# Kernel tuning notes

Hardware: AMD Instinct MI355X
Metric: run time of the kernel (lower is better)

The kernel has to match this reference:

```python
import jax, jax.numpy as jnp
import numpy as np

DT = 0.1       # time separation between grid points (forward dt arg default)
UT = 0.1       # stationary-mode time constant
K_IN, K_OUT, K_STATE = 8, 4, 128
PRE_LEN, FWD_LEN, BATCH = 64, 128, 4096


def setup_inputs() -> dict:
    key = jax.random.key(0)
    ks = jax.random.split(key, 16)
    H = K_STATE
    s = 0.05  # small init keeps the 128-step integration numerically tame
    d = {}
    d['pre_x'] = jax.random.normal(ks[0], (PRE_LEN, BATCH, K_IN), jnp.float32)
    d['pre_y'] = jax.random.normal(ks[1], (PRE_LEN, BATCH, K_OUT), jnp.float32)
    d['forward_x'] = jax.random.normal(ks[2], (FWD_LEN, BATCH, K_IN), jnp.float32)
    # encoder nn.GRU (1 layer), torch gate order r,z,n
    d['W_ih'] = jax.random.normal(ks[3], (3 * H, K_IN + K_OUT), jnp.float32) * s
    d['W_hh'] = jax.random.normal(ks[4], (3 * H, H), jnp.float32) * s
    d['b_ih'] = jax.random.normal(ks[5], (3 * H,), jnp.float32) * s
    d['b_hh'] = jax.random.normal(ks[6], (3 * H,), jnp.float32) * s
    # expand_input: Linear(k_in, k_state) + Tanh
    d['W_e'] = jax.random.normal(ks[7], (H, K_IN), jnp.float32) * s
    d['b_e'] = jax.random.normal(ks[8], (H,), jnp.float32) * s
    # ODE GRU cell (BasicCell with net_type='GRU'): input size = k_state
    d['Wc_ih'] = jax.random.normal(ks[9], (3 * H, H), jnp.float32) * s
    d['Wc_hh'] = jax.random.normal(ks[10], (3 * H, H), jnp.float32) * s
    d['bc_ih'] = jax.random.normal(ks[11], (3 * H,), jnp.float32) * s
    d['bc_hh'] = jax.random.normal(ks[12], (3 * H,), jnp.float32) * s
    # fc: Linear(H, 2H, bias=False) -> Tanh -> Linear(2H, k_out, bias=False)
    d['W1'] = jax.random.normal(ks[13], (2 * H, H), jnp.float32) * s
    d['W2'] = jax.random.normal(ks[14], (K_OUT, 2 * H), jnp.float32) * s
    return d


def _gru_cell(x, h, Wi, Wh, bi, bh):
    gi = x @ Wi.T + bi
    gh = h @ Wh.T + bh
    ir, iz, inn = jnp.split(gi, 3, axis=-1)
    hr, hz, hn = jnp.split(gh, 3, axis=-1)
    r = jax.nn.sigmoid(ir + hr)
    z = jax.nn.sigmoid(iz + hz)
    n = jnp.tanh(inn + r * hn)
    return (1.0 - z) * n + z * h


def reference(pre_x, pre_y, forward_x, W_ih, W_hh, b_ih, b_hh, W_e, b_e,
              Wc_ih, Wc_hh, bc_ih, bc_hh, W1, W2):
    H = W_hh.shape[1]
    # ---- GRU encoder over [pre_x, pre_y], take final hidden state ----
    enc_in = jnp.concatenate([pre_x, pre_y], axis=2)  # [Tp, B, k_in+k_out]
    h0 = jnp.zeros((enc_in.shape[1], H), enc_in.dtype)

    def enc_step(h, x):
        return _gru_cell(x, h, W_ih, W_hh, b_ih, b_hh), None

    hn, _ = jax.lax.scan(enc_step, h0, enc_in)  # [B, H]

    # ---- natural cubic spline of the control input over the grid ----
    L = forward_x.shape[0]
    hs = DT
    ys = jnp.concatenate([pre_x[-1:], forward_x], axis=0)  # [L+1, B, k_in]
    rhs = 6.0 * (ys[:-2] - 2.0 * ys[1:-1] + ys[2:]) / (hs * hs)  # [L-1, ...]
    nin = L - 1
    A = 4.0 * jnp.eye(nin) + jnp.eye(nin, k=1) + jnp.eye(nin, k=-1)
    Minner = jnp.linalg.solve(A, rhs.reshape(nin, -1)).reshape(rhs.shape)
    zpad = jnp.zeros_like(ys[:1])
    M = jnp.concatenate([zpad, Minner, zpad], axis=0)  # 2nd derivs, [L+1,B,k_in]

    def u(t):
        i = jnp.clip(jnp.floor(t / hs).astype(jnp.int32), 0, L - 1)
        t0 = i.astype(ys.dtype) * hs
        a = (t0 + hs - t) / hs
        b = (t - t0) / hs
        yi, yi1 = jnp.take(ys, i, axis=0), jnp.take(ys, i + 1, axis=0)
        Mi, Mi1 = jnp.take(M, i, axis=0), jnp.take(M, i + 1, axis=0)
        return a * yi + b * yi1 + ((a ** 3 - a) * Mi + (b ** 3 - b) * Mi1) * (hs * hs) / 6.0

    # ---- ODE system: stationary GRU-cell dynamics ----
    def f(t, y):
        x = jnp.tanh(u(t) @ W_e.T + b_e)
        return (_gru_cell(x, y, Wc_ih, Wc_hh, bc_ih, bc_hh) - y) / UT

    # ---- fixed-grid RK4 (torchdiffeq method='rk4', one step per interval) ----
    def rk4(y, t0):
        k1 = f(t0, y)
        k2 = f(t0 + hs / 2, y + (hs / 2) * k1)
        k3 = f(t0 + hs / 2, y + (hs / 2) * k2)
        k4 = f(t0 + hs, y + hs * k3)
        yn = y + (hs / 6.0) * (k1 + 2 * k2 + 2 * k3 + k4)
        return yn, yn

    t_starts = jnp.arange(L, dtype=ys.dtype) * hs
    _, traj = jax.lax.scan(rk4, hn, t_starts)  # [L, B, H]

    # ---- output head: Linear -> Tanh -> Linear (no bias) ----
    return jnp.tanh(traj @ W1.T) @ W2.T  # [L, B, k_out]
```

## Files before the change

### kernel.cpp

```cpp
#include <hip/hip_runtime.h>
#include <math.h>

#define NB    4096
#define NH    128
#define NKIN  8
#define NKOUT 4
#define NTP   64
#define NL    128
#define BKIN  (NB*NKIN)

typedef __attribute__((ext_vector_type(8))) short short8;
typedef __attribute__((ext_vector_type(4))) float f32x4;

__device__ __forceinline__ short f2bf(float f) {
    union { float f; unsigned u; } v; v.f = f;
    unsigned u = v.u;
    unsigned r = (u + 0x7fffu + ((u >> 16) & 1u)) >> 16;
    return (short)r;
}
__device__ __forceinline__ float sigf(float x)   { return __builtin_amdgcn_rcpf(1.0f + __expf(-x)); }
__device__ __forceinline__ float tanhf_(float x) { return 1.0f - 2.0f*__builtin_amdgcn_rcpf(1.0f + __expf(2.0f*x)); }

__global__ void spline_um_kernel(const float* __restrict__ pre_x,
                                 const float* __restrict__ fx,
                                 float* __restrict__ UM)
{
    __shared__ float cp[128];
    if (threadIdx.x == 0) {
        float c = 0.f;
        for (int j = 1; j <= 127; ++j) { c = 1.0f/(4.0f - c); cp[j] = c; }
    }
    __syncthreads();
    int col = blockIdx.x*256 + threadIdx.x;
    const float r6 = 6.0f/(0.1f*0.1f);
    const float KK = 0.01f/16.0f;
    float y0 = pre_x[(size_t)(NTP-1)*BKIN + col];
    float y1 = fx[col];
    float d = 0.f;
    for (int j = 1; j <= 127; ++j) {
        float y2 = fx[(size_t)j*BKIN + col];
        float r  = r6*(y0 - 2.f*y1 + y2);
        d = (r - d)*cp[j];
        UM[(size_t)j*BKIN + col] = d;
        y0 = y1; y1 = y2;
    }
    float xn  = 0.f;
    float yj1 = fx[(size_t)127*BKIN + col];
    for (int j = 127; j >= 1; --j) {
        float dj = UM[(size_t)j*BKIN + col];
        float x  = dj - cp[j]*xn;
        float yj = fx[(size_t)(j-1)*BKIN + col];
        UM[(size_t)j*BKIN + col] = 0.5f*(yj + yj1) - KK*(x + xn);
        xn = x; yj1 = yj;
    }
    float ys0 = pre_x[(size_t)(NTP-1)*BKIN + col];
    UM[col] = 0.5f*(ys0 + yj1) - KK*xn;
}

__global__ void prep_frags(const float* __restrict__ W1, const float* __restrict__ W2,
                           short* __restrict__ w1f, short* __restrict__ w2f)
{
    int tid = threadIdx.x;
    for (int idx = tid; idx < 16*4*64*8; idx += 256) {
        int j = idx & 7, lane = (idx >> 3) & 63, fc = idx >> 9;
        int t = fc >> 2, c = fc & 3;
        int n = t*16 + (lane & 15);
        int k = c*32 + (lane >> 4)*8 + j;
        w1f[idx] = f2bf(W1[n*NH + k]);
    }
    for (int idx = tid; idx < 8*64*8; idx += 256) {
        int j = idx & 7, lane = (idx >> 3) & 63, c = idx >> 9;
        int m = lane & 15;
        int k = c*32 + (lane >> 4)*8 + j;
        w2f[idx] = (m < NKOUT) ? f2bf(W2[m*2*NH + k]) : (short)0;
    }
}

__device__ __forceinline__ void gemm12(const short* base, const short8 (&B)[3][4], f32x4 (&c)[3])
{
    #pragma unroll
    for (int kc = 0; kc < 4; ++kc) {
        short8 a = *(const short8*)(base + kc*32);
        #pragma unroll
        for (int g = 0; g < 3; ++g)
            c[g] = __builtin_amdgcn_mfma_f32_16x16x32_bf16(a, B[g][kc], c[g], 0, 0, 0);
    }
}

__device__ __forceinline__ void writeA(short* buf, int stride, int col, int quad, f32x4 v)
{
    #pragma unroll
    for (int r = 0; r < 4; ++r) buf[(quad*4 + r)*stride + col] = f2bf(v[r]);
}

__device__ __forceinline__ void gateK(const f32x4 (&gi)[3], const f32x4 (&gh)[3],
                                      const f32x4& yin, float brz, float bzz,
                                      float bin_, float bhn_, f32x4& K)
{
    #pragma unroll
    for (int r = 0; r < 4; ++r) {
        float rg = sigf(gi[0][r] + gh[0][r] + brz);
        float zg = sigf(gi[1][r] + gh[1][r] + bzz);
        float ng = tanhf_(gi[2][r] + bin_ + rg*(gh[2][r] + bhn_));
        K[r] = (1.0f - zg)*(ng - yin[r]);
    }
}

__global__ void __launch_bounds__(512, 2)
fused_kernel(const float* __restrict__ pre_x, const float* __restrict__ pre_y,
             const float* __restrict__ fx,
             const float* __restrict__ W_ih, const float* __restrict__ W_hh,
             const float* __restrict__ b_ih, const float* __restrict__ b_hh,
             const float* __restrict__ W_e,  const float* __restrict__ b_e,
             const float* __restrict__ Wc_ih,const float* __restrict__ Wc_hh,
             const float* __restrict__ bc_ih,const float* __restrict__ bc_hh,
             const float* __restrict__ UM,   const short* __restrict__ w1f,
             const short* __restrict__ w2f,  float* __restrict__ out)
{
    __shared__ __align__(16) short Yb [16*136];
    __shared__ __align__(16) short E0 [16*136];
    __shared__ __align__(16) short E1 [16*136];
    __shared__ __align__(16) short XMb[16*136];
    __shared__ __align__(16) short X1b[16*136];
    __shared__ __align__(16) short UMb[16*40];
    __shared__ __align__(16) short U1b[16*40];
    __shared__ __align__(16) short OB [16*264];

    const int tid  = threadIdx.x;
    const int w    = tid >> 6;
    const int lane = tid & 63;
    const int quad = lane >> 4;
    const int m    = lane & 15;
    const int hcol = w*16 + m;
    const int b0   = blockIdx.x * 16;
    const f32x4 z4 = {0.f, 0.f, 0.f, 0.f};

    for (int i = tid; i < 2176; i += 512) Yb[i] = 0;
    for (int i = tid; i < 640;  i += 512) { UMb[i] = 0; U1b[i] = 0; }

    short8 Bhh[3][4], Bih_c[3][4];
    #pragma unroll
    for (int g = 0; g < 3; ++g)
        #pragma unroll
        for (int c = 0; c < 4; ++c) {
            int n = g*NH + hcol, kb = c*32 + quad*8;
            short8 f1, f2;
            #pragma unroll
            for (int j = 0; j < 8; ++j) {
                f1[j] = f2bf(Wc_hh[n*NH + kb + j]);
                f2[j] = f2bf(Wc_ih[n*NH + kb + j]);
            }
            Bhh[g][c] = f1; Bih_c[g][c] = f2;
        }
    short8 Ehh[3][4];
    #pragma unroll
    for (int g = 0; g < 3; ++g)
        #pragma unroll
        for (int c = 0; c < 4; ++c) {
            int n = g*NH + hcol, kb = c*32 + quad*8;
            short8 f1;
            #pragma unroll
            for (int j = 0; j < 8; ++j) f1[j] = f2bf(W_hh[n*NH + kb + j]);
            Ehh[g][c] = f1;
        }
    short8 Eih[3];
    #pragma unroll
    for (int g = 0; g < 3; ++g) {
        short8 f1;
        #pragma unroll
        for (int j = 0; j < 8; ++j) {
            int k = quad*8 + j;
            f1[j] = (k < 12) ? f2bf(W_ih[(g*NH + hcol)*12 + k]) : (short)0;
        }
        Eih[g] = f1;
    }
    short8 Bexp;
    #pragma unroll
    for (int j = 0; j < 8; ++j) {
        int k = quad*8 + j;
        Bexp[j] = (k < NKIN) ? f2bf(W_e[hcol*NKIN + k]) : (short)0;
    }
    const float be   = b_e[hcol];
    const float brz  = bc_ih[hcol]        + bc_hh[hcol];
    const float bzz  = bc_ih[NH + hcol]   + bc_hh[NH + hcol];
    const float bin_ = bc_ih[2*NH + hcol];
    const float bhn_ = bc_hh[2*NH + hcol];
    const float erz  = b_ih[hcol]         + b_hh[hcol];
    const float ezz  = b_ih[NH + hcol]    + b_hh[NH + hcol];
    const float ein_ = b_ih[2*NH + hcol];
    const float ehn_ = b_hh[2*NH + hcol];

    f32x4 y = z4;

    const int eb = tid / 12, ek = tid - eb*12;
    float encv = 0.f;
    if (tid < 192)
        encv = (ek < NKIN) ? pre_x[((size_t)0*NB + b0 + eb)*NKIN + ek]
                           : pre_y[((size_t)0*NB + b0 + eb)*NKOUT + (ek - NKIN)];
    __syncthreads();
    for (int t = 0; t < NTP; ++t) {
        if (tid < 192) {
            UMb[eb*40 + ek] = f2bf(encv);
            if (t + 1 < NTP)
                encv = (ek < NKIN) ? pre_x[((size_t)(t+1)*NB + b0 + eb)*NKIN + ek]
                                   : pre_y[((size_t)(t+1)*NB + b0 + eb)*NKOUT + (ek - NKIN)];
        }
        __syncthreads();
        f32x4 gi[3] = {z4, z4, z4};
        {
            short8 a = *(const short8*)(UMb + m*40 + quad*8);
            #pragma unroll
            for (int g = 0; g < 3; ++g)
                gi[g] = __builtin_amdgcn_mfma_f32_16x16x32_bf16(a, Eih[g], gi[g], 0, 0, 0);
        }
        f32x4 gh[3] = {z4, z4, z4};
        gemm12(Yb + m*136 + quad*8, Ehh, gh);
        f32x4 K;
        gateK(gi, gh, y, erz, ezz, ein_, ehn_, K);
        #pragma unroll
        for (int r = 0; r < 4; ++r) y[r] += K[r];
        __syncthreads();
        writeA(Yb, 136, hcol, quad, y);
    }
    if (tid < 64) UMb[(tid >> 2)*40 + 8 + (tid & 3)] = 0;

    const int sb = tid >> 3, sk = tid & 7;
    const size_t scol = (size_t)(b0 + sb)*NKIN + sk;
    if (tid < 128) UMb[sb*40 + sk] = f2bf(pre_x[(size_t)(NTP-1)*BKIN + scol]);
    __syncthreads();
    f32x4 gi0[3] = {z4, z4, z4};
    {
        short8 a = *(const short8*)(UMb + m*40 + quad*8);
        f32x4 c0 = z4;
        c0 = __builtin_amdgcn_mfma_f32_16x16x32_bf16(a, Bexp, c0, 0, 0, 0);
        f32x4 xv;
        #pragma unroll
        for (int r = 0; r < 4; ++r) xv[r] = tanhf_(c0[r] + be);
        writeA(XMb, 136, hcol, quad, xv);
    }
    __syncthreads();
    gemm12(XMb + m*136 + quad*8, Bih_c, gi0);

    float fxv = 0.f, umv = 0.f;
    if (tid < 128) { fxv = fx[scol]; umv = UM[scol]; }

    const short8* W1F = (const short8*)w1f;
    const short8* W2F = (const short8*)w2f;

    for (int st = 0; st < NL; ++st) {
        if (tid < 128) {
            U1b[sb*40 + sk] = f2bf(fxv);
            UMb[sb*40 + sk] = f2bf(umv);
        }
        __syncthreads();
        f32x4 xmv, x1v;
        {
            short8 am = *(const short8*)(UMb + m*40 + quad*8);
            short8 a1 = *(const short8*)(U1b + m*40 + quad*8);
            f32x4 cm = z4, c1 = z4;
            cm = __builtin_amdgcn_mfma_f32_16x16x32_bf16(am, Bexp, cm, 0, 0, 0);
            c1 = __builtin_amdgcn_mfma_f32_16x16x32_bf16(a1, Bexp, c1, 0, 0, 0);
            #pragma unroll
            for (int r = 0; r < 4; ++r) {
                xmv[r] = tanhf_(cm[r] + be);
                x1v[r] = tanhf_(c1[r] + be);
            }
        }
        writeA(XMb, 136, hcol, quad, xmv);
        writeA(X1b, 136, hcol, quad, x1v);
        if (tid < 128 && st + 1 < NL) {
            fxv = fx[(size_t)(st+1)*BKIN + scol];
            umv = UM[(size_t)(st+1)*BKIN + scol];
        }
        __syncthreads();
        f32x4 gim[3] = {z4, z4, z4}, gi1[3] = {z4, z4, z4};
        gemm12(XMb + m*136 + quad*8, Bih_c, gim);
        gemm12(X1b + m*136 + quad*8, Bih_c, gi1);
        f32x4 gh[3] = {z4, z4, z4};
        gemm12(Yb + m*136 + quad*8, Bhh, gh);
        f32x4 K1, Ks, ye;
        gateK(gi0, gh, y, brz, bzz, bin_, bhn_, K1);
        #pragma unroll
        for (int r = 0; r < 4; ++r) { Ks[r] = K1[r]; ye[r] = y[r] + 0.5f*K1[r]; }
        writeA(E0, 136, hcol, quad, ye);
        __syncthreads();
        gh[0] = z4; gh[1] = z4; gh[2] = z4;
        gemm12(E0 + m*136 + quad*8, Bhh, gh);
        f32x4 K2;
        gateK(gim, gh, ye, brz, bzz, bin_, bhn_, K2);
        #pragma unroll
        for (int r = 0; r < 4; ++r) { Ks[r] += 2.f*K2[r]; ye[r] = y[r] + 0.5f*K2[r]; }
        writeA(E1, 136, hcol, quad, ye);
        __syncthreads();
        gh[0] = z4; gh[1] = z4; gh[2] = z4;
        gemm12(E1 + m*136 + quad*8, Bhh, gh);
        f32x4 K3;
        gateK(gim, gh, ye, brz, bzz, bin_, bhn_, K3);
        #pragma unroll
        for (int r = 0; r < 4; ++r) { Ks[r] += 2.f*K3[r]; ye[r] = y[r] + K3[r]; }
        writeA(E0, 136, hcol, quad, ye);
        __syncthreads();
        gh[0] = z4; gh[1] = z4; gh[2] = z4;
        gemm12(E0 + m*136 + quad*8, Bhh, gh);
        f32x4 K4;
        gateK(gi1, gh, ye, brz, bzz, bin_, bhn_, K4);
        #pragma unroll
        for (int r = 0; r < 4; ++r) y[r] += (1.0f/6.0f)*(Ks[r] + K4[r]);
        gi0[0] = gi1[0]; gi0[1] = gi1[1]; gi0[2] = gi1[2];
        writeA(Yb, 136, hcol, quad, y);
        __syncthreads();
        {
            f32x4 o0 = z4, o1 = z4;
            #pragma unroll
            for (int kc = 0; kc < 4; ++kc) {
                short8 a  = *(const short8*)(Yb + m*136 + quad*8 + kc*32);
                short8 bA = W1F[((w    )*4 + kc)*64 + lane];
                short8 bB = W1F[((w + 8)*4 + kc)*64 + lane];
                o0 = __builtin_amdgcn_mfma_f32_16x16x32_bf16(a, bA, o0, 0, 0, 0);
                o1 = __builtin_amdgcn_mfma_f32_16x16x32_bf16(a, bB, o1, 0, 0, 0);
            }
            #pragma unroll
            for (int r = 0; r < 4; ++r) {
                OB[(quad*4 + r)*264 + hcol]       = f2bf(tanhf_(o0[r]));
                OB[(quad*4 + r)*264 + 128 + hcol] = f2bf(tanhf_(o1[r]));
            }
        }
        __syncthreads();
        if (w == 0) {
            f32x4 oc = z4;
            #pragma unroll
            for (int c = 0; c < 8; ++c) {
                short8 bo = *(const short8*)(OB + m*264 + c*32 + quad*8);
                short8 aw = W2F[c*64 + lane];
                oc = __builtin_amdgcn_mfma_f32_16x16x32_bf16(aw, bo, oc, 0, 0, 0);
            }
            if (quad == 0)
                *(f32x4*)(out + ((size_t)st*NB + b0 + m)*NKOUT) = oc;
        }
    }
}

extern "C" void kernel_launch(void* const* d_in, const int* in_sizes, int n_in,
                              void* d_out, int out_size, void* d_ws, size_t ws_size,
                              hipStream_t stream)
{
    const float* pre_x = (const float*)d_in[0];
    const float* pre_y = (const float*)d_in[1];
    const float* fx    = (const float*)d_in[2];
    const float* W_ih  = (const float*)d_in[3];
    const float* W_hh  = (const float*)d_in[4];
    const float* b_ih  = (const float*)d_in[5];
    const float* b_hh  = (const float*)d_in[6];
    const float* W_e   = (const float*)d_in[7];
    const float* b_e   = (const float*)d_in[8];
    const float* Wc_ih = (const float*)d_in[9];
    const float* Wc_hh = (const float*)d_in[10];
    const float* bc_ih = (const float*)d_in[11];
    const float* bc_hh = (const float*)d_in[12];
    const float* W1    = (const float*)d_in[13];
    const float* W2    = (const float*)d_in[14];
    float* out = (float*)d_out;

    float* UM  = (float*)d_ws;
    short* w1f = (short*)((char*)d_ws + (size_t)NL*NB*NKIN*4);
    short* w2f = w1f + 16*4*64*8;

    prep_frags<<<dim3(1), dim3(256), 0, stream>>>(W1, W2, w1f, w2f);
    spline_um_kernel<<<dim3((NB*NKIN)/256), dim3(256), 0, stream>>>(pre_x, fx, UM);
    fused_kernel<<<dim3(NB/16), dim3(512), 0, stream>>>(
        pre_x, pre_y, fx, W_ih, W_hh, b_ih, b_hh, W_e, b_e,
        Wc_ih, Wc_hh, bc_ih, bc_hh, UM, w1f, w2f, out);
}
```

Baseline: 790.9 us.

## Restructure ODE loop: transposed MFMA, folded biases/log2e, fewer barriers, rotated output warp

After: 798.3 us. Within noise of the previous version (+0.9%).

```diff
diff --git a/kernel.cpp b/kernel.cpp
--- a/kernel.cpp
+++ b/kernel.cpp
@@ -8,18 +8,37 @@
 #define NTP   64
 #define NL    128
 #define BKIN  (NB*NKIN)
+#define LOG2E 1.44269504088896340736f
 
 typedef __attribute__((ext_vector_type(8))) short short8;
 typedef __attribute__((ext_vector_type(4))) float f32x4;
+
+#if __has_builtin(__builtin_amdgcn_exp2f)
+#define EXP2F __builtin_amdgcn_exp2f
+#else
+#define EXP2F exp2f
+#endif
 
 __device__ __forceinline__ short f2bf(float f) {
     union { float f; unsigned u; } v; v.f = f;
     unsigned u = v.u;
-    unsigned r = (u + 0x7fffu + ((u >> 16) & 1u)) >> 16;
-    return (short)r;
-}
-__device__ __forceinline__ float sigf(float x)   { return __builtin_amdgcn_rcpf(1.0f + __expf(-x)); }
-__device__ __forceinline__ float tanhf_(float x) { return 1.0f - 2.0f*__builtin_amdgcn_rcpf(1.0f + __expf(2.0f*x)); }
+    return (short)((u + 0x7fffu + ((u >> 16) & 1u)) >> 16);
+}
+__device__ __forceinline__ unsigned pkbf2(float a, float b) {
+#if __has_builtin(__builtin_amdgcn_cvt_pk_bf16_f32)
+    auto p = __builtin_amdgcn_cvt_pk_bf16_f32(a, b);
+    unsigned q; __builtin_memcpy(&q, &p, 4); return q;
+#else
+    union { float f; unsigned u; } x, y; x.f = a; y.f = b;
+    unsigned ua = (x.u + 0x7fffu + ((x.u >> 16) & 1u)) >> 16;
+    unsigned ub = (y.u + 0x7fffu + ((y.u >> 16) & 1u)) & 0xffff0000u;
+    return ua | ub;
+#endif
+}
+__device__ __forceinline__ void st4(short* dst, const f32x4& v) {
+    uint2 q; q.x = pkbf2(v[0], v[1]); q.y = pkbf2(v[2], v[3]);
+    *(uint2*)dst = q;
+}
 
 __global__ void spline_um_kernel(const float* __restrict__ pre_x,
                                  const float* __restrict__ fx,
@@ -31,7 +50,7 @@
         for (int j = 1; j <= 127; ++j) { c = 1.0f/(4.0f - c); cp[j] = c; }
     }
     __syncthreads();
-    int col = blockIdx.x*256 + threadIdx.x;
+    int col = blockIdx.x*128 + threadIdx.x;
     const float r6 = 6.0f/(0.1f*0.1f);
     const float KK = 0.01f/16.0f;
     float y0 = pre_x[(size_t)(NTP-1)*BKIN + col];
@@ -62,47 +81,39 @@
 {
     int tid = threadIdx.x;
     for (int idx = tid; idx < 16*4*64*8; idx += 256) {
-        int j = idx & 7, lane = (idx >> 3) & 63, fc = idx >> 9;
-        int t = fc >> 2, c = fc & 3;
-        int n = t*16 + (lane & 15);
-        int k = c*32 + (lane >> 4)*8 + j;
-        w1f[idx] = f2bf(W1[n*NH + k]);
+        int j = idx & 7, lane = (idx >> 3) & 63, kc = (idx >> 9) & 3, t = idx >> 11;
+        int row = t*16 + (lane & 15);
+        int k   = kc*32 + (lane >> 4)*8 + j;
+        w1f[idx] = f2bf(2.0f*LOG2E*W1[row*NH + k]);
     }
     for (int idx = tid; idx < 8*64*8; idx += 256) {
-        int j = idx & 7, lane = (idx >> 3) & 63, c = idx >> 9;
+        int j = idx & 7, lane = (idx >> 3) & 63, kc = idx >> 9;
         int m = lane & 15;
-        int k = c*32 + (lane >> 4)*8 + j;
+        int k = kc*32 + (lane >> 4)*8 + j;
         w2f[idx] = (m < NKOUT) ? f2bf(W2[m*2*NH + k]) : (short)0;
     }
 }
 
-__device__ __forceinline__ void gemm12(const short* base, const short8 (&B)[3][4], f32x4 (&c)[3])
+__device__ __forceinline__ void gemmB(const short* bp, const short8 (&A)[3][4], f32x4 (&acc)[3])
 {
     #pragma unroll
     for (int kc = 0; kc < 4; ++kc) {
-        short8 a = *(const short8*)(base + kc*32);
+        short8 b = *(const short8*)(bp + kc*32);
         #pragma unroll
         for (int g = 0; g < 3; ++g)
-            c[g] = __builtin_amdgcn_mfma_f32_16x16x32_bf16(a, B[g][kc], c[g], 0, 0, 0);
-    }
-}
-
-__device__ __forceinline__ void writeA(short* buf, int stride, int col, int quad, f32x4 v)
-{
-    #pragma unroll
-    for (int r = 0; r < 4; ++r) buf[(quad*4 + r)*stride + col] = f2bf(v[r]);
+            acc[g] = __builtin_amdgcn_mfma_f32_16x16x32_bf16(A[g][kc], b, acc[g], 0, 0, 0);
+    }
 }
 
 __device__ __forceinline__ void gateK(const f32x4 (&gi)[3], const f32x4 (&gh)[3],
-                                      const f32x4& yin, float brz, float bzz,
-                                      float bin_, float bhn_, f32x4& K)
+                                      const f32x4& yin, f32x4& K)
 {
     #pragma unroll
     for (int r = 0; r < 4; ++r) {
-        float rg = sigf(gi[0][r] + gh[0][r] + brz);
-        float zg = sigf(gi[1][r] + gh[1][r] + bzz);
-        float ng = tanhf_(gi[2][r] + bin_ + rg*(gh[2][r] + bhn_));
-        K[r] = (1.0f - zg)*(ng - yin[r]);
+        float rg = __builtin_amdgcn_rcpf(1.0f + EXP2F(gi[0][r] + gh[0][r]));
+        float zg = __builtin_amdgcn_rcpf(1.0f + EXP2F(gi[1][r] + gh[1][r]));
+        float tg = 1.0f - 2.0f*__builtin_amdgcn_rcpf(1.0f + EXP2F(gi[2][r] + rg*gh[2][r]));
+        K[r] = (1.0f - zg)*(tg - yin[r]);
     }
 }
 
@@ -117,226 +128,261 @@
              const float* __restrict__ UM,   const short* __restrict__ w1f,
              const short* __restrict__ w2f,  float* __restrict__ out)
 {
-    __shared__ __align__(16) short Yb [16*136];
+    __shared__ __align__(16) short yT [16*136];
     __shared__ __align__(16) short E0 [16*136];
     __shared__ __align__(16) short E1 [16*136];
-    __shared__ __align__(16) short XMb[16*136];
-    __shared__ __align__(16) short X1b[16*136];
+    __shared__ __align__(16) short xmT[16*136];
+    __shared__ __align__(16) short x1T[16*136];
     __shared__ __align__(16) short UMb[16*40];
     __shared__ __align__(16) short U1b[16*40];
-    __shared__ __align__(16) short OB [16*264];
+    __shared__ __align__(16) short oT [16*264];
 
     const int tid  = threadIdx.x;
     const int w    = tid >> 6;
     const int lane = tid & 63;
     const int quad = lane >> 4;
     const int m    = lane & 15;
-    const int hcol = w*16 + m;
+    const int hq   = w*16 + quad*4;
     const int b0   = blockIdx.x * 16;
     const f32x4 z4 = {0.f, 0.f, 0.f, 0.f};
 
-    for (int i = tid; i < 2176; i += 512) Yb[i] = 0;
-    for (int i = tid; i < 640;  i += 512) { UMb[i] = 0; U1b[i] = 0; }
-
-    short8 Bhh[3][4], Bih_c[3][4];
+    for (int i = tid; i < 16*136; i += 512) yT[i] = 0;
+    for (int i = tid; i < 16*40;  i += 512) { UMb[i] = 0; U1b[i] = 0; }
+
+    const float scg[3] = {-LOG2E, -LOG2E, 2.0f*LOG2E};
+
+    short8 Ahh[3][4], Aih[3][4];
     #pragma unroll
     for (int g = 0; g < 3; ++g)
         #pragma unroll
         for (int c = 0; c < 4; ++c) {
-            int n = g*NH + hcol, kb = c*32 + quad*8;
-            short8 f1, f2;
-            #pragma unroll
-            for (int j = 0; j < 8; ++j) {
-                f1[j] = f2bf(Wc_hh[n*NH + kb + j]);
-                f2[j] = f2bf(Wc_ih[n*NH + kb + j]);
-            }
-            Bhh[g][c] = f1; Bih_c[g][c] = f2;
-        }
-    short8 Ehh[3][4];
-    #pragma unroll
-    for (int g = 0; g < 3; ++g)
-        #pragma unroll
-        for (int c = 0; c < 4; ++c) {
-            int n = g*NH + hcol, kb = c*32 + quad*8;
-            short8 f1;
-            #pragma unroll
-            for (int j = 0; j < 8; ++j) f1[j] = f2bf(W_hh[n*NH + kb + j]);
-            Ehh[g][c] = f1;
-        }
-    short8 Eih[3];
-    #pragma unroll
-    for (int g = 0; g < 3; ++g) {
-        short8 f1;
-        #pragma unroll
-        for (int j = 0; j < 8; ++j) {
-            int k = quad*8 + j;
-            f1[j] = (k < 12) ? f2bf(W_ih[(g*NH + hcol)*12 + k]) : (short)0;
-        }
-        Eih[g] = f1;
-    }
-    short8 Bexp;
+            const float* ph = Wc_hh + (size_t)(g*NH + w*16 + m)*NH + c*32 + quad*8;
+            const float* pi = Wc_ih + (size_t)(g*NH + w*16 + m)*NH + c*32 + quad*8;
+            short8 fh, fi;
+            #pragma unroll
+            for (int j = 0; j < 8; ++j) { fh[j] = f2bf(scg[g]*ph[j]); fi[j] = f2bf(scg[g]*pi[j]); }
+            Ahh[g][c] = fh; Aih[g][c] = fi;
+        }
+    short8 Aexp;
     #pragma unroll
     for (int j = 0; j < 8; ++j) {
         int k = quad*8 + j;
-        Bexp[j] = (k < NKIN) ? f2bf(W_e[hcol*NKIN + k]) : (short)0;
-    }
-    const float be   = b_e[hcol];
-    const float brz  = bc_ih[hcol]        + bc_hh[hcol];
-    const float bzz  = bc_ih[NH + hcol]   + bc_hh[NH + hcol];
-    const float bin_ = bc_ih[2*NH + hcol];
-    const float bhn_ = bc_hh[2*NH + hcol];
-    const float erz  = b_ih[hcol]         + b_hh[hcol];
-    const float ezz  = b_ih[NH + hcol]    + b_hh[NH + hcol];
-    const float ein_ = b_ih[2*NH + hcol];
-    const float ehn_ = b_hh[2*NH + hcol];
+        Aexp[j] = (k < NKIN) ? f2bf(2.0f*LOG2E*W_e[(w*16 + m)*NKIN + k]) : (short)0;
+    }
+    f32x4 brz4, bzz4, bgn4, bin4, be4;
+    #pragma unroll
+    for (int r = 0; r < 4; ++r) {
+        int h = hq + r;
+        brz4[r] = -LOG2E*(bc_ih[h]      + bc_hh[h]);
+        bzz4[r] = -LOG2E*(bc_ih[NH + h] + bc_hh[NH + h]);
+        bgn4[r] = 2.0f*LOG2E*bc_hh[2*NH + h];
+        bin4[r] = 2.0f*LOG2E*bc_ih[2*NH + h];
+        be4[r]  = 2.0f*LOG2E*b_e[h];
+    }
 
     f32x4 y = z4;
 
-    const int eb = tid / 12, ek = tid - eb*12;
-    float encv = 0.f;
-    if (tid < 192)
-        encv = (ek < NKIN) ? pre_x[((size_t)0*NB + b0 + eb)*NKIN + ek]
-                           : pre_y[((size_t)0*NB + b0 + eb)*NKOUT + (ek - NKIN)];
-    __syncthreads();
-    for (int t = 0; t < NTP; ++t) {
-        if (tid < 192) {
-            UMb[eb*40 + ek] = f2bf(encv);
-            if (t + 1 < NTP)
-                encv = (ek < NKIN) ? pre_x[((size_t)(t+1)*NB + b0 + eb)*NKIN + ek]
-                                   : pre_y[((size_t)(t+1)*NB + b0 + eb)*NKOUT + (ek - NKIN)];
-        }
-        __syncthreads();
-        f32x4 gi[3] = {z4, z4, z4};
-        {
-            short8 a = *(const short8*)(UMb + m*40 + quad*8);
-            #pragma unroll
-            for (int g = 0; g < 3; ++g)
-                gi[g] = __builtin_amdgcn_mfma_f32_16x16x32_bf16(a, Eih[g], gi[g], 0, 0, 0);
-        }
-        f32x4 gh[3] = {z4, z4, z4};
-        gemm12(Yb + m*136 + quad*8, Ehh, gh);
-        f32x4 K;
-        gateK(gi, gh, y, erz, ezz, ein_, ehn_, K);
-        #pragma unroll
-        for (int r = 0; r < 4; ++r) y[r] += K[r];
-        __syncthreads();
-        writeA(Yb, 136, hcol, quad, y);
-    }
+    {
+        short8 Ehh[3][4];
+        #pragma unroll
+        for (int g = 0; g < 3; ++g)
+            #pragma unroll
+            for (int c = 0; c < 4; ++c) {
+                const float* ph = W_hh + (size_t)(g*NH + w*16 + m)*NH + c*32 + quad*8;
+                short8 fh;
+                #pragma unroll
+                for (int j = 0; j < 8; ++j) fh[j] = f2bf(scg[g]*ph[j]);
+                Ehh[g][c] = fh;
+            }
+        short8 Eih[3];
+        #pragma unroll
+        for (int g = 0; g < 3; ++g) {
+            short8 f1;
+            #pragma unroll
+            for (int j = 0; j < 8; ++j) {
+                int k = quad*8 + j;
+                f1[j] = (k < 12) ? f2bf(scg[g]*W_ih[(size_t)(g*NH + w*16 + m)*12 + k]) : (short)0;
+            }
+            Eih[g] = f1;
+        }
+        f32x4 erz4, ezz4, egn4, ein4;
+        #pragma unroll
+        for (int r = 0; r < 4; ++r) {
+            int h = hq + r;
+            erz4[r] = -LOG2E*(b_ih[h]      + b_hh[h]);
+            ezz4[r] = -LOG2E*(b_ih[NH + h] + b_hh[NH + h]);
+            egn4[r] = 2.0f*LOG2E*b_hh[2*NH + h];
+            ein4[r] = 2.0f*LOG2E*b_ih[2*NH + h];
+        }
+        const int eb = tid / 12, ek = tid - eb*12;
+        float encv = 0.f;
+        if (tid < 192)
+            encv = (ek < NKIN) ? pre_x[((size_t)0*NB + b0 + eb)*NKIN + ek]
+                               : pre_y[((size_t)0*NB + b0 + eb)*NKOUT + (ek - NKIN)];
+        __syncthreads();
+        for (int t = 0; t < NTP; ++t) {
+            if (tid < 192) {
+                UMb[eb*40 + ek] = f2bf(encv);
+                if (t + 1 < NTP)
+                    encv = (ek < NKIN) ? pre_x[((size_t)(t+1)*NB + b0 + eb)*NKIN + ek]
+                                       : pre_y[((size_t)(t+1)*NB + b0 + eb)*NKOUT + (ek - NKIN)];
+            }
+            __syncthreads();
+            f32x4 gi[3] = {z4, z4, ein4};
+            {
+                short8 b = *(const short8*)(UMb + m*40 + quad*8);
+                #pragma unroll
+                for (int g = 0; g < 3; ++g)
+                    gi[g] = __builtin_amdgcn_mfma_f32_16x16x32_bf16(Eih[g], b, gi[g], 0, 0, 0);
+            }
+            f32x4 gh[3] = {erz4, ezz4, egn4};
+            gemmB(yT + m*136 + quad*8, Ehh, gh);
+            f32x4 K;
+            gateK(gi, gh, y, K);
+            #pragma unroll
+            for (int r = 0; r < 4; ++r) y[r] += K[r];
+            __syncthreads();
+            st4(yT + m*136 + hq, y);
+        }
+    }
+
     if (tid < 64) UMb[(tid >> 2)*40 + 8 + (tid & 3)] = 0;
-
     const int sb = tid >> 3, sk = tid & 7;
     const size_t scol = (size_t)(b0 + sb)*NKIN + sk;
     if (tid < 128) UMb[sb*40 + sk] = f2bf(pre_x[(size_t)(NTP-1)*BKIN + scol]);
     __syncthreads();
-    f32x4 gi0[3] = {z4, z4, z4};
     {
-        short8 a = *(const short8*)(UMb + m*40 + quad*8);
-        f32x4 c0 = z4;
-        c0 = __builtin_amdgcn_mfma_f32_16x16x32_bf16(a, Bexp, c0, 0, 0, 0);
+        short8 b = *(const short8*)(UMb + m*40 + quad*8);
+        f32x4 c0 = be4;
+        c0 = __builtin_amdgcn_mfma_f32_16x16x32_bf16(Aexp, b, c0, 0, 0, 0);
         f32x4 xv;
         #pragma unroll
-        for (int r = 0; r < 4; ++r) xv[r] = tanhf_(c0[r] + be);
-        writeA(XMb, 136, hcol, quad, xv);
+        for (int r = 0; r < 4; ++r)
+            xv[r] = 1.0f - 2.0f*__builtin_amdgcn_rcpf(1.0f + EXP2F(c0[r]));
+        st4(xmT + m*136 + hq, xv);
     }
     __syncthreads();
-    gemm12(XMb + m*136 + quad*8, Bih_c, gi0);
-
+    f32x4 gi0[3] = {z4, z4, bin4};
+    gemmB(xmT + m*136 + quad*8, Aih, gi0);
+    if (tid < 128) { UMb[sb*40 + sk] = f2bf(UM[scol]); U1b[sb*40 + sk] = f2bf(fx[scol]); }
+    __syncthreads();
+    {
+        short8 bm = *(const short8*)(UMb + m*40 + quad*8);
+        short8 b1 = *(const short8*)(U1b + m*40 + quad*8);
+        f32x4 cm = be4, c1 = be4;
+        cm = __builtin_amdgcn_mfma_f32_16x16x32_bf16(Aexp, bm, cm, 0, 0, 0);
+        c1 = __builtin_amdgcn_mfma_f32_16x16x32_bf16(Aexp, b1, c1, 0, 0, 0);
+        f32x4 xm, x1;
+        #pragma unroll
+        for (int r = 0; r < 4; ++r) {
+            xm[r] = 1.0f - 2.0f*__builtin_amdgcn_rcpf(1.0f + EXP2F(cm[r]));
+            x1[r] = 1.0f - 2.0f*__builtin_amdgcn_rcpf(1.0f + EXP2F(c1[r]));
+        }
+        st4(xmT + m*136 + hq, xm);
+        st4(x1T + m*136 + hq, x1);
+    }
+    __syncthreads();
+    f32x4 gim[3] = {z4, z4, bin4}, gi1[3] = {z4, z4, bin4};
+    gemmB(xmT + m*136 + quad*8, Aih, gim);
+    gemmB(x1T + m*136 + quad*8, Aih, gi1);
     float fxv = 0.f, umv = 0.f;
-    if (tid < 128) { fxv = fx[scol]; umv = UM[scol]; }
-
-    const short8* W1F = (const short8*)w1f;
-    const short8* W2F = (const short8*)w2f;
+    if (tid < 128) { fxv = fx[BKIN + scol]; umv = UM[BKIN + scol]; }
 
     for (int st = 0; st < NL; ++st) {
-        if (tid < 128) {
-            U1b[sb*40 + sk] = f2bf(fxv);
-            UMb[sb*40 + sk] = f2bf(umv);
-        }
-        __syncthreads();
-        f32x4 xmv, x1v;
+        f32x4 gh[3] = {brz4, bzz4, bgn4};
+        gemmB(yT + m*136 + quad*8, Ahh, gh);
+        f32x4 K, Ks, ye;
+        gateK(gi0, gh, y, K);
+        #pragma unroll
+        for (int r = 0; r < 4; ++r) { Ks[r] = K[r]; ye[r] = y[r] + 0.5f*K[r]; }
+        st4(E0 + m*136 + hq, ye);
+        __syncthreads();
+        gh[0] = brz4; gh[1] = bzz4; gh[2] = bgn4;
+        gemmB(E0 + m*136 + quad*8, Ahh, gh);
+        gateK(gim, gh, ye, K);
+        #pragma unroll
+        for (int r = 0; r < 4; ++r) { Ks[r] += 2.f*K[r]; ye[r] = y[r] + 0.5f*K[r]; }
+        st4(E1 + m*136 + hq, ye);
+        __syncthreads();
+        gh[0] = brz4; gh[1] = bzz4; gh[2] = bgn4;
+        gemmB(E1 + m*136 + quad*8, Ahh, gh);
+        gateK(gim, gh, ye, K);
+        #pragma unroll
+        for (int r = 0; r < 4; ++r) { Ks[r] += 2.f*K[r]; ye[r] = y[r] + K[r]; }
+        st4(E0 + m*136 + hq, ye);
+        __syncthreads();
+        gh[0] = brz4; gh[1] = bzz4; gh[2] = bgn4;
+        gemmB(E0 + m*136 + quad*8, Ahh, gh);
+        gateK(gi1, gh, ye, K);
+        #pragma unroll
+        for (int r = 0; r < 4; ++r) y[r] += (1.0f/6.0f)*(Ks[r] + K[r]);
+        st4(yT + m*136 + hq, y);
+        if (tid < 128) { UMb[sb*40 + sk] = f2bf(umv); U1b[sb*40 + sk] = f2bf(fxv); }
+        short8 a1f[2][4];
+        #pragma unroll
+        for (int kc = 0; kc < 4; ++kc) {
+            a1f[0][kc] = *(const short8*)(w1f + (size_t)((w*4      + kc)*64 + lane)*8);
+            a1f[1][kc] = *(const short8*)(w1f + (size_t)(((w+8)*4 + kc)*64 + lane)*8);
+        }
+        __syncthreads();
         {
-            short8 am = *(const short8*)(UMb + m*40 + quad*8);
-            short8 a1 = *(const short8*)(U1b + m*40 + quad*8);
-            f32x4 cm = z4, c1 = z4;
-            cm = __builtin_amdgcn_mfma_f32_16x16x32_bf16(am, Bexp, cm, 0, 0, 0);
-            c1 = __builtin_amdgcn_mfma_f32_16x16x32_bf16(a1, Bexp, c1, 0, 0, 0);
+            short8 bm = *(const short8*)(UMb + m*40 + quad*8);
+            short8 b1 = *(const short8*)(U1b + m*40 + quad*8);
+            f32x4 cm = be4, c1 = be4;
+            cm = __builtin_amdgcn_mfma_f32_16x16x32_bf16(Aexp, bm, cm, 0, 0, 0);
+            c1 = __builtin_amdgcn_mfma_f32_16x16x32_bf16(Aexp, b1, c1, 0, 0, 0);
+            f32x4 xm, x1;
             #pragma unroll
             for (int r = 0; r < 4; ++r) {
-                xmv[r] = tanhf_(cm[r] + be);
-                x1v[r] = tanhf_(c1[r] + be);
-            }
-        }
-        writeA(XMb, 136, hcol, quad, xmv);
-        writeA(X1b, 136, hcol, quad, x1v);
-        if (tid < 128 && st + 1 < NL) {
-            fxv = fx[(size_t)(st+1)*BKIN + scol];
-            umv = UM[(size_t)(st+1)*BKIN + scol];
-        }
-        __syncthreads();
-        f32x4 gim[3] = {z4, z4, z4}, gi1[3] = {z4, z4, z4};
-        gemm12(XMb + m*136 + quad*8, Bih_c, gim);
-        gemm12(X1b + m*136 + quad*8, Bih_c, gi1);
-        f32x4 gh[3] = {z4, z4, z4};
-        gemm12(Yb + m*136 + quad*8, Bhh, gh);
-        f32x4 K1, Ks, ye;
-        gateK(gi0, gh, y, brz, bzz, bin_, bhn_, K1);
-        #pragma unroll
-        for (int r = 0; r < 4; ++r) { Ks[r] = K1[r]; ye[r] = y[r] + 0.5f*K1[r]; }
-        writeA(E0, 136, hcol, quad, ye);
-        __syncthreads();
-        gh[0] = z4; gh[1] = z4; gh[2] = z4;
-        gemm12(E0 + m*136 + quad*8, Bhh, gh);
-        f32x4 K2;
-        gateK(gim, gh, ye, brz, bzz, bin_, bhn_, K2);
-        #pragma unroll
-        for (int r = 0; r < 4; ++r) { Ks[r] += 2.f*K2[r]; ye[r] = y[r] + 0.5f*K2[r]; }
-        writeA(E1, 136, hcol, quad, ye);
-        __syncthreads();
-        gh[0] = z4; gh[1] = z4; gh[2] = z4;
-        gemm12(E1 + m*136 + quad*8, Bhh, gh);
-        f32x4 K3;
-        gateK(gim, gh, ye, brz, bzz, bin_, bhn_, K3);
-        #pragma unroll
-        for (int r = 0; r < 4; ++r) { Ks[r] += 2.f*K3[r]; ye[r] = y[r] + K3[r]; }
-        writeA(E0, 136, hcol, quad, ye);
-        __syncthreads();
-        gh[0] = z4; gh[1] = z4; gh[2] = z4;
-        gemm12(E0 + m*136 + quad*8, Bhh, gh);
-        f32x4 K4;
-        gateK(gi1, gh, ye, brz, bzz, bin_, bhn_, K4);
-        #pragma unroll
-        for (int r = 0; r < 4; ++r) y[r] += (1.0f/6.0f)*(Ks[r] + K4[r]);
-        gi0[0] = gi1[0]; gi0[1] = gi1[1]; gi0[2] = gi1[2];
-        writeA(Yb, 136, hcol, quad, y);
-        __syncthreads();
+                xm[r] = 1.0f - 2.0f*__builtin_amdgcn_rcpf(1.0f + EXP2F(cm[r]));
+                x1[r] = 1.0f - 2.0f*__builtin_amdgcn_rcpf(1.0f + EXP2F(c1[r]));
+            }
+            st4(xmT + m*136 + hq, xm);
+            st4(x1T + m*136 + hq, x1);
+        }
         {
             f32x4 o0 = z4, o1 = z4;
             #pragma unroll
             for (int kc = 0; kc < 4; ++kc) {
-                short8 a  = *(const short8*)(Yb + m*136 + quad*8 + kc*32);
-                short8 bA = W1F[((w    )*4 + kc)*64 + lane];
-                short8 bB = W1F[((w + 8)*4 + kc)*64 + lane];
-                o0 = __builtin_amdgcn_mfma_f32_16x16x32_bf16(a, bA, o0, 0, 0, 0);
-                o1 = __builtin_amdgcn_mfma_f32_16x16x32_bf16(a, bB, o1, 0, 0, 0);
-            }
+                short8 b = *(const short8*)(yT + m*136 + quad*8 + kc*32);
+                o0 = __builtin_amdgcn_mfma_f32_16x16x32_bf16(a1f[0][kc], b, o0, 0, 0, 0);
+                o1 = __builtin_amdgcn_mfma_f32_16x16x32_bf16(a1f[1][kc], b, o1, 0, 0, 0);
+            }
+            f32x4 t0, t1;
             #pragma unroll
             for (int r = 0; r < 4; ++r) {
-                OB[(quad*4 + r)*264 + hcol]       = f2bf(tanhf_(o0[r]));
-                OB[(quad*4 + r)*264 + 128 + hcol] = f2bf(tanhf_(o1[r]));
-            }
-        }
-        __syncthreads();
-        if (w == 0) {
+                t0[r] = 1.0f - 2.0f*__builtin_amdgcn_rcpf(1.0f + EXP2F(o0[r]));
+                t1[r] = 1.0f - 2.0f*__builtin_amdgcn_rcpf(1.0f + EXP2F(o1[r]));
+            }
+            st4(oT + m*264 + w*16     + quad*4, t0);
+            st4(oT + m*264 + (w+8)*16 + quad*4, t1);
+        }
+        if (tid < 128) {
+            if (st + 2 < NL) { fxv = fx[(size_t)(st+2)*BKIN + scol]; umv = UM[(size_t)(st+2)*BKIN + scol]; }
+            else             { fxv = 0.f; umv = 0.f; }
+        }
+        short8 a2f[8];
+        if (w == (st & 7)) {
+            #pragma unroll
+            for (int kc = 0; kc < 8; ++kc)
+                a2f[kc] = *(const short8*)(w2f + (size_t)(kc*64 + lane)*8);
+        }
+        __syncthreads();
+        if (w == (st & 7)) {
             f32x4 oc = z4;
             #pragma unroll
-            for (int c = 0; c < 8; ++c) {
-                short8 bo = *(const short8*)(OB + m*264 + c*32 + quad*8);
-                short8 aw = W2F[c*64 + lane];
-                oc = __builtin_amdgcn_mfma_f32_16x16x32_bf16(aw, bo, oc, 0, 0, 0);
+            for (int kc = 0; kc < 8; ++kc) {
+                short8 b = *(const short8*)(oT + m*264 + kc*32 + quad*8);
+                oc = __builtin_amdgcn_mfma_f32_16x16x32_bf16(a2f[kc], b, oc, 0, 0, 0);
             }
             if (quad == 0)
                 *(f32x4*)(out + ((size_t)st*NB + b0 + m)*NKOUT) = oc;
         }
+        gi0[0] = gi1[0]; gi0[1] = gi1[1]; gi0[2] = gi1[2];
+        gim[0] = z4; gim[1] = z4; gim[2] = bin4;
+        gi1[0] = z4; gi1[1] = z4; gi1[2] = bin4;
+        gemmB(xmT + m*136 + quad*8, Aih, gim);
+        gemmB(x1T + m*136 + quad*8, Aih, gi1);
     }
 }
 
@@ -366,7 +412,7 @@
     short* w2f = w1f + 16*4*64*8;
 
     prep_frags<<<dim3(1), dim3(256), 0, stream>>>(W1, W2, w1f, w2f);
-    spline_um_kernel<<<dim3((NB*NKIN)/256), dim3(256), 0, stream>>>(pre_x, fx, UM);
+    spline_um_kernel<<<dim3((NB*NKIN)/128), dim3(128), 0, stream>>>(pre_x, fx, UM);
     fused_kernel<<<dim3(NB/16), dim3(512), 0, stream>>>(
         pre_x, pre_y, fx, W_ih, W_hh, b_ih, b_hh, W_e, b_e,
         Wc_ih, Wc_hh, bc_ih, bc_hh, UM, w1f, w2f, out);
```
